# Kernel tuning notes

Measured on AMD Instinct MI355X. Metric: run time of the kernel, lower is better.

Reference implementation:

```python
import jax, jax.numpy as jnp
import numpy as np

NUM_TAGS = 128
NUM_FEATURES = 500000
B, T, F = 64, 512, 8


def setup_inputs() -> dict:
    key = jax.random.key(0)
    ks = jax.random.split(key, 6)
    feats = jax.random.randint(ks[0], (B, T, F), 0, NUM_FEATURES)
    tags = jax.random.randint(ks[1], (B, T), 0, NUM_TAGS)
    # original init: uniform(-0.01, 0.01)
    state_weights = jax.random.uniform(ks[2], (NUM_TAGS, NUM_FEATURES), minval=-0.01, maxval=0.01, dtype=jnp.float32)
    transitions = jax.random.uniform(ks[3], (NUM_TAGS, NUM_TAGS), minval=-0.01, maxval=0.01, dtype=jnp.float32)
    start_transitions = jax.random.uniform(ks[4], (NUM_TAGS,), minval=-0.01, maxval=0.01, dtype=jnp.float32)
    end_transitions = jax.random.uniform(ks[5], (NUM_TAGS,), minval=-0.01, maxval=0.01, dtype=jnp.float32)
    return dict(feats=feats, tags=tags, state_weights=state_weights,
                transitions=transitions, start_transitions=start_transitions,
                end_transitions=end_transitions)


def reference(feats, tags, state_weights, transitions, start_transitions, end_transitions):
    """Batched CRF negative log-likelihood per sentence: logZ - gold_score. Returns [B]."""
    # emissions[b,t,k] = sum_f state_weights[k, feats[b,t,f]]  (emissions_for_sentence)
    emissions = jnp.take(state_weights, feats, axis=1).sum(-1)   # [K,B,T]
    emissions = jnp.moveaxis(emissions, 0, -1)                    # [B,T,K]

    # log_partition: forward algorithm over T via scan
    alpha0 = start_transitions[None, :] + emissions[:, 0]         # [B,K]

    def step(alpha, em_t):
        # scores[b,i,j] = alpha[b,i] + transitions[i,j]
        scores = alpha[:, :, None] + transitions[None, :, :]
        return jax.nn.logsumexp(scores, axis=1) + em_t, None

    em_rest = jnp.moveaxis(emissions[:, 1:], 1, 0)                # [T-1,B,K]
    alphaT, _ = jax.lax.scan(step, alpha0, em_rest)
    log_z = jax.nn.logsumexp(alphaT + end_transitions[None, :], axis=1)   # [B]

    # gold_score, vectorized over batch
    em_gold = jnp.take_along_axis(emissions, tags[..., None], axis=2)[..., 0].sum(axis=1)  # [B]
    trans_gold = transitions[tags[:, :-1], tags[:, 1:]].sum(axis=1)                        # [B]
    gold = start_transitions[tags[:, 0]] + end_transitions[tags[:, -1]] + em_gold + trans_gold

    return log_z - gold
```

## Files before the change

### kernel.cpp

```cpp
#include <hip/hip_runtime.h>

#define NUM_TAGS 128
#define NUM_FEATS 500000
#define BB 64
#define TT 512
#define FF 8

#define SWT_BYTES 128000000ull
#define EM_BYTES  16777216ull
#define NEED_FULL (SWT_BYTES + EM_BYTES)

typedef __attribute__((ext_vector_type(8))) short short8;
typedef __attribute__((ext_vector_type(4))) float float4v;

__device__ inline unsigned short f2bf(float f) {
  unsigned u = __float_as_uint(f);
  return (unsigned short)((u + 0x7fffu + ((u >> 16) & 1u)) >> 16);
}
__device__ inline float bf2f(unsigned short h) {
  return __uint_as_float(((unsigned)h) << 16);
}

__global__ __launch_bounds__(256) void transpose_kernel(
    const float* __restrict__ sw, unsigned short* __restrict__ swT) {
  __shared__ float tile[32][129];
  const int f0 = blockIdx.x * 32;
  const int t = threadIdx.x;
  const int fi = t & 31, kb = t >> 5;
#pragma unroll
  for (int it = 0; it < 16; ++it) {
    int k = kb + it * 8;
    tile[fi][k] = sw[(size_t)k * NUM_FEATS + f0 + fi];
  }
  __syncthreads();
  const int kp = (t & 63) * 2, fo = t >> 6;
#pragma unroll
  for (int it = 0; it < 8; ++it) {
    int f2 = fo + it * 4;
    unsigned v = (unsigned)f2bf(tile[f2][kp]) |
                 ((unsigned)f2bf(tile[f2][kp + 1]) << 16);
    *(unsigned*)&swT[(size_t)(f0 + f2) * NUM_TAGS + kp] = v;
  }
}

__global__ __launch_bounds__(128) void gather_t_kernel(
    const int* __restrict__ feats, const unsigned short* __restrict__ swT,
    float* __restrict__ em_exp) {
  const int token = blockIdx.x;
  const int k = threadIdx.x;
  const int* f = feats + token * FF;
  float s = 0.f;
#pragma unroll
  for (int i = 0; i < FF; ++i) s += bf2f(swT[(size_t)f[i] * NUM_TAGS + k]);
  em_exp[(size_t)token * NUM_TAGS + k] = __expf(s);
}

__global__ __launch_bounds__(128) void gather_f_kernel(
    const int* __restrict__ feats, const float* __restrict__ sw,
    float* __restrict__ em_exp) {
  const int token = blockIdx.x;
  const int k = threadIdx.x;
  const int* f = feats + token * FF;
  const float* row = sw + (size_t)k * NUM_FEATS;
  float s = 0.f;
#pragma unroll
  for (int i = 0; i < FF; ++i) s += row[f[i]];
  em_exp[(size_t)token * NUM_TAGS + k] = __expf(s);
}

#define NB 16
#define LROW 136
#define LBUF (NB * LROW)

__global__ __launch_bounds__(256, 1) void fwd_kernel(
    const float* __restrict__ em_exp, const int* __restrict__ tags,
    const float* __restrict__ trans, const float* __restrict__ startT,
    const float* __restrict__ endT, float* __restrict__ out) {
  __shared__ __align__(16) unsigned short abuf[2][LBUF];
  __shared__ float red[16][17];

  const int tid = threadIdx.x;
  const int bl = tid & 15;
  const int h = (tid >> 4) & 3;
  const int w = tid >> 6;
  const int bg = blockIdx.x * NB + bl;

  short8 afrag[2][4];
#pragma unroll
  for (int mt = 0; mt < 2; ++mt) {
    const int j = (2 * w + mt) * 16 + bl;
#pragma unroll
    for (int kc = 0; kc < 4; ++kc) {
      short8 a;
#pragma unroll
      for (int jj = 0; jj < 8; ++jj) {
        int i = kc * 32 + h * 8 + jj;
        a[jj] = (short)f2bf(__expf(trans[i * NUM_TAGS + j]) * 0.0078125f);
      }
      afrag[mt][kc] = a;
    }
  }

  const float* emb = em_exp + (size_t)bg * TT * NUM_TAGS;

  {
    const int jc = tid >> 4, j0 = jc * 8;
#pragma unroll
    for (int jj = 0; jj < 8; ++jj)
      abuf[0][bl * LROW + j0 + jj] =
          f2bf(__expf(startT[j0 + jj]) * emb[j0 + jj]);
  }
  __syncthreads();

  float4v ev[2];
#pragma unroll
  for (int mt = 0; mt < 2; ++mt) {
    int j0 = (2 * w + mt) * 16 + h * 4;
    ev[mt] = *(const float4v*)&emb[(size_t)NUM_TAGS + j0];
  }

  for (int t = 1; t < TT; ++t) {
    const unsigned short* cur = abuf[(t - 1) & 1];
    unsigned short* nxt = abuf[t & 1];

    short8 bfrag[4];
#pragma unroll
    for (int kc = 0; kc < 4; ++kc)
      bfrag[kc] = *(const short8*)&cur[bl * LROW + kc * 32 + h * 8];

    float4v acc0 = {0.f, 0.f, 0.f, 0.f}, acc1 = {0.f, 0.f, 0.f, 0.f};
#pragma unroll
    for (int kc = 0; kc < 4; ++kc) {
      acc0 = __builtin_amdgcn_mfma_f32_16x16x32_bf16(afrag[0][kc], bfrag[kc], acc0, 0, 0, 0);
      acc1 = __builtin_amdgcn_mfma_f32_16x16x32_bf16(afrag[1][kc], bfrag[kc], acc1, 0, 0, 0);
    }

    float4v e0 = ev[0], e1 = ev[1];
    if (t + 1 < TT) {
#pragma unroll
      for (int mt = 0; mt < 2; ++mt) {
        int j0 = (2 * w + mt) * 16 + h * 4;
        ev[mt] = *(const float4v*)&emb[(size_t)(t + 1) * NUM_TAGS + j0];
      }
    }
    {
      int j0 = (2 * w + 0) * 16 + h * 4;
      uint2 u;
      u.x = (unsigned)f2bf(acc0[0] * e0[0]) | ((unsigned)f2bf(acc0[1] * e0[1]) << 16);
      u.y = (unsigned)f2bf(acc0[2] * e0[2]) | ((unsigned)f2bf(acc0[3] * e0[3]) << 16);
      *(uint2*)&nxt[bl * LROW + j0] = u;
    }
    {
      int j0 = (2 * w + 1) * 16 + h * 4;
      uint2 u;
      u.x = (unsigned)f2bf(acc1[0] * e1[0]) | ((unsigned)f2bf(acc1[1] * e1[1]) << 16);
      u.y = (unsigned)f2bf(acc1[2] * e1[2]) | ((unsigned)f2bf(acc1[3] * e1[3]) << 16);
      *(uint2*)&nxt[bl * LROW + j0] = u;
    }
    __syncthreads();
  }

  {
    const int jc = tid >> 4, j0 = jc * 8;
    const unsigned short* fin = abuf[(TT - 1) & 1];
    float val = 0.f;
#pragma unroll
    for (int jj = 0; jj < 8; ++jj)
      val += bf2f(fin[bl * LROW + j0 + jj]) * __expf(endT[j0 + jj]);
    red[jc][bl] = val;
  }
  __syncthreads();
  float logzv = 0.f;
  if (tid < 16) {
    float s = 0.f;
#pragma unroll
    for (int q = 0; q < 16; ++q) s += red[q][tid];
    logzv = __logf(s) + 511.0f * 7.0f * 0.69314718055994531f;
  }
  __syncthreads();

  {
    const int seg = tid >> 4;
    const int* tb = tags + (size_t)bg * TT;
    float g = 0.f;
    for (int t = seg * 32; t < seg * 32 + 32; ++t) {
      int tg = tb[t];
      g += __logf(emb[(size_t)t * NUM_TAGS + tg]);
      if (t < TT - 1) g += trans[tg * NUM_TAGS + tb[t + 1]];
    }
    if (seg == 0) g += startT[tb[0]];
    if (seg == 15) g += endT[tb[TT - 1]];
    red[seg][bl] = g;
  }
  __syncthreads();
  if (tid < 16) {
    float s = 0.f;
#pragma unroll
    for (int q = 0; q < 16; ++q) s += red[q][tid];
    out[blockIdx.x * NB + tid] = logzv - s;
  }
}

extern "C" void kernel_launch(void* const* d_in, const int* in_sizes, int n_in,
                              void* d_out, int out_size, void* d_ws, size_t ws_size,
                              hipStream_t stream) {
  const int* feats = (const int*)d_in[0];
  const int* tags = (const int*)d_in[1];
  const float* sw = (const float*)d_in[2];
  const float* trans = (const float*)d_in[3];
  const float* startT = (const float*)d_in[4];
  const float* endT = (const float*)d_in[5];
  float* out = (float*)d_out;

  if (ws_size >= NEED_FULL) {
    unsigned short* swT = (unsigned short*)d_ws;
    float* em_exp = (float*)((char*)d_ws + SWT_BYTES);
    transpose_kernel<<<NUM_FEATS / 32, 256, 0, stream>>>(sw, swT);
    gather_t_kernel<<<BB * TT, 128, 0, stream>>>(feats, swT, em_exp);
    fwd_kernel<<<BB / NB, 256, 0, stream>>>(em_exp, tags, trans, startT, endT, out);
  } else {
    float* em_exp = (float*)d_ws;
    gather_f_kernel<<<BB * TT, 128, 0, stream>>>(feats, sw, em_exp);
    fwd_kernel<<<BB / NB, 256, 0, stream>>>(em_exp, tags, trans, startT, endT, out);
  }
}
```

Measured before the change: 633.9 us.

## Store emissions as bf16, precompute gold score in gather, widen transpose tiles

Emission storage moves from fp32 to bf16, which halves the traffic for writing and reading the emission buffer. The gold emission term is now taken from the raw sums inside the gather kernel, and a separate small kernel computes the gold transition term, so the serial forward kernel no longer does log lookups at the end. The transpose kernel switches to 128-feature tiles with float4 loads and converts to bf16 before staging in LDS. The gather kernel packs two tags per lane with 8 tokens per block, and the forward loop uses a cheaper bf16 rounding built on perm, which adds a little precision loss.

```diff
diff --git a/kernel.cpp b/kernel.cpp
--- a/kernel.cpp
+++ b/kernel.cpp
@@ -7,8 +7,10 @@
 #define FF 8
 
 #define SWT_BYTES 128000000ull
-#define EM_BYTES  16777216ull
-#define NEED_FULL (SWT_BYTES + EM_BYTES)
+#define EM_BYTES  (64ull * 512 * 128 * 2)
+#define GEP_BYTES (4096ull * 4)
+#define GTR_BYTES (64ull * 4)
+#define NEED_FULL (SWT_BYTES + EM_BYTES + GEP_BYTES + GTR_BYTES)
 
 typedef __attribute__((ext_vector_type(8))) short short8;
 typedef __attribute__((ext_vector_type(4))) float float4v;
@@ -21,69 +23,141 @@
   return __uint_as_float(((unsigned)h) << 16);
 }
 
+__global__ __launch_bounds__(256) void gold_trans_kernel(
+    const int* __restrict__ tags, const float* __restrict__ trans,
+    const float* __restrict__ startT, const float* __restrict__ endT,
+    float* __restrict__ gold_tr) {
+  const int b = blockIdx.x;
+  const int* tb = tags + (size_t)b * TT;
+  float g = 0.f;
+  for (int t = threadIdx.x; t < TT - 1; t += 256)
+    g += trans[tb[t] * NUM_TAGS + tb[t + 1]];
+  if (threadIdx.x == 0) g += startT[tb[0]] + endT[tb[TT - 1]];
+#pragma unroll
+  for (int m = 32; m > 0; m >>= 1) g += __shfl_xor(g, m, 64);
+  __shared__ float r[4];
+  if ((threadIdx.x & 63) == 0) r[threadIdx.x >> 6] = g;
+  __syncthreads();
+  if (threadIdx.x == 0) gold_tr[b] = r[0] + r[1] + r[2] + r[3];
+}
+
 __global__ __launch_bounds__(256) void transpose_kernel(
     const float* __restrict__ sw, unsigned short* __restrict__ swT) {
-  __shared__ float tile[32][129];
-  const int f0 = blockIdx.x * 32;
+#define TS 136
+  __shared__ unsigned short tile[128 * TS];
+  const int f0 = blockIdx.x * 128;
   const int t = threadIdx.x;
-  const int fi = t & 31, kb = t >> 5;
-#pragma unroll
-  for (int it = 0; it < 16; ++it) {
-    int k = kb + it * 8;
-    tile[fi][k] = sw[(size_t)k * NUM_FEATS + f0 + fi];
-  }
-  __syncthreads();
-  const int kp = (t & 63) * 2, fo = t >> 6;
-#pragma unroll
-  for (int it = 0; it < 8; ++it) {
-    int f2 = fo + it * 4;
-    unsigned v = (unsigned)f2bf(tile[f2][kp]) |
-                 ((unsigned)f2bf(tile[f2][kp + 1]) << 16);
-    *(unsigned*)&swT[(size_t)(f0 + f2) * NUM_TAGS + kp] = v;
-  }
-}
-
-__global__ __launch_bounds__(128) void gather_t_kernel(
+  const int c = t & 31, kr = t >> 5;
+#pragma unroll
+  for (int p = 0; p < 16; ++p) {
+    int k = kr + 8 * p;
+    int f = f0 + 4 * c;
+    if (f < NUM_FEATS) {
+      float4 v = *(const float4*)&sw[(size_t)k * NUM_FEATS + f];
+      uint2 o;
+      o.x = (unsigned)f2bf(v.x) | ((unsigned)f2bf(v.y) << 16);
+      o.y = (unsigned)f2bf(v.z) | ((unsigned)f2bf(v.w) << 16);
+      *(uint2*)&tile[k * TS + 4 * c] = o;
+    }
+  }
+  __syncthreads();
+  const int c2 = t & 31, fr = t >> 5;
+#pragma unroll
+  for (int p = 0; p < 16; ++p) {
+    int f = fr + 8 * p;
+    if (f0 + f < NUM_FEATS) {
+      uint2 o;
+      o.x = (unsigned)tile[(4 * c2 + 0) * TS + f] |
+            ((unsigned)tile[(4 * c2 + 1) * TS + f] << 16);
+      o.y = (unsigned)tile[(4 * c2 + 2) * TS + f] |
+            ((unsigned)tile[(4 * c2 + 3) * TS + f] << 16);
+      *(uint2*)&swT[(size_t)(f0 + f) * NUM_TAGS + 4 * c2] = o;
+    }
+  }
+#undef TS
+}
+
+__global__ __launch_bounds__(512) void gather_kernel(
     const int* __restrict__ feats, const unsigned short* __restrict__ swT,
-    float* __restrict__ em_exp) {
-  const int token = blockIdx.x;
-  const int k = threadIdx.x;
-  const int* f = feats + token * FF;
-  float s = 0.f;
-#pragma unroll
-  for (int i = 0; i < FF; ++i) s += bf2f(swT[(size_t)f[i] * NUM_TAGS + k]);
-  em_exp[(size_t)token * NUM_TAGS + k] = __expf(s);
-}
-
-__global__ __launch_bounds__(128) void gather_f_kernel(
+    unsigned short* __restrict__ em, const int* __restrict__ tags,
+    float* __restrict__ gold_ep) {
+  const int w = threadIdx.x >> 6, lane = threadIdx.x & 63;
+  const int token = blockIdx.x * 8 + w;
+  const int* f = feats + (size_t)token * FF;
+  float s0 = 0.f, s1 = 0.f;
+#pragma unroll
+  for (int i = 0; i < FF; ++i) {
+    unsigned u = *(const unsigned*)&swT[(size_t)f[i] * NUM_TAGS + 2 * lane];
+    s0 += __uint_as_float(u << 16);
+    s1 += __uint_as_float(u & 0xFFFF0000u);
+  }
+  unsigned lo = f2bf(__expf(s0));
+  unsigned hi = f2bf(__expf(s1));
+  *(unsigned*)&em[(size_t)token * NUM_TAGS + 2 * lane] = lo | (hi << 16);
+
+  int tg = tags[token];
+  float c = (2 * lane == tg) ? s0 : ((2 * lane + 1 == tg) ? s1 : 0.f);
+#pragma unroll
+  for (int m = 32; m > 0; m >>= 1) c += __shfl_xor(c, m, 64);
+  __shared__ float part[8];
+  if (lane == 0) part[w] = c;
+  __syncthreads();
+  if (threadIdx.x == 0) {
+    float s = 0.f;
+#pragma unroll
+    for (int i = 0; i < 8; ++i) s += part[i];
+    gold_ep[blockIdx.x] = s;
+  }
+}
+
+__global__ __launch_bounds__(512) void gather_f_kernel(
     const int* __restrict__ feats, const float* __restrict__ sw,
-    float* __restrict__ em_exp) {
-  const int token = blockIdx.x;
-  const int k = threadIdx.x;
-  const int* f = feats + token * FF;
-  const float* row = sw + (size_t)k * NUM_FEATS;
-  float s = 0.f;
-#pragma unroll
-  for (int i = 0; i < FF; ++i) s += row[f[i]];
-  em_exp[(size_t)token * NUM_TAGS + k] = __expf(s);
+    unsigned short* __restrict__ em, const int* __restrict__ tags,
+    float* __restrict__ gold_ep) {
+  const int w = threadIdx.x >> 6, lane = threadIdx.x & 63;
+  const int token = blockIdx.x * 8 + w;
+  const int* f = feats + (size_t)token * FF;
+  float s0 = 0.f, s1 = 0.f;
+#pragma unroll
+  for (int i = 0; i < FF; ++i) {
+    s0 += sw[(size_t)(2 * lane) * NUM_FEATS + f[i]];
+    s1 += sw[(size_t)(2 * lane + 1) * NUM_FEATS + f[i]];
+  }
+  unsigned lo = f2bf(__expf(s0));
+  unsigned hi = f2bf(__expf(s1));
+  *(unsigned*)&em[(size_t)token * NUM_TAGS + 2 * lane] = lo | (hi << 16);
+
+  int tg = tags[token];
+  float c = (2 * lane == tg) ? s0 : ((2 * lane + 1 == tg) ? s1 : 0.f);
+#pragma unroll
+  for (int m = 32; m > 0; m >>= 1) c += __shfl_xor(c, m, 64);
+  __shared__ float part[8];
+  if (lane == 0) part[w] = c;
+  __syncthreads();
+  if (threadIdx.x == 0) {
+    float s = 0.f;
+#pragma unroll
+    for (int i = 0; i < 8; ++i) s += part[i];
+    gold_ep[blockIdx.x] = s;
+  }
 }
 
 #define NB 16
 #define LROW 136
-#define LBUF (NB * LROW)
 
 __global__ __launch_bounds__(256, 1) void fwd_kernel(
-    const float* __restrict__ em_exp, const int* __restrict__ tags,
-    const float* __restrict__ trans, const float* __restrict__ startT,
-    const float* __restrict__ endT, float* __restrict__ out) {
-  __shared__ __align__(16) unsigned short abuf[2][LBUF];
+    const unsigned short* __restrict__ em, const float* __restrict__ trans,
+    const float* __restrict__ startT, const float* __restrict__ endT,
+    const float* __restrict__ gold_tr, const float* __restrict__ gold_ep,
+    float* __restrict__ out) {
+  __shared__ __align__(16) unsigned short alds[2][NB * LROW];
   __shared__ float red[16][17];
+  __shared__ float redz[16];
 
   const int tid = threadIdx.x;
-  const int bl = tid & 15;
-  const int h = (tid >> 4) & 3;
-  const int w = tid >> 6;
-  const int bg = blockIdx.x * NB + bl;
+  const int w = tid >> 6, lane = tid & 63;
+  const int bl = lane & 15, h = lane >> 4;
+  const int b0 = blockIdx.x * NB;
 
   short8 afrag[2][4];
 #pragma unroll
@@ -101,27 +175,35 @@
     }
   }
 
-  const float* emb = em_exp + (size_t)bg * TT * NUM_TAGS;
+  const unsigned short* emb = em + (size_t)(b0 + bl) * TT * NUM_TAGS;
 
   {
-    const int jc = tid >> 4, j0 = jc * 8;
-#pragma unroll
-    for (int jj = 0; jj < 8; ++jj)
-      abuf[0][bl * LROW + j0 + jj] =
-          f2bf(__expf(startT[j0 + jj]) * emb[j0 + jj]);
-  }
-  __syncthreads();
-
-  float4v ev[2];
-#pragma unroll
-  for (int mt = 0; mt < 2; ++mt) {
-    int j0 = (2 * w + mt) * 16 + h * 4;
-    ev[mt] = *(const float4v*)&emb[(size_t)NUM_TAGS + j0];
-  }
+    const int bl2 = tid & 15, jc = tid >> 4;
+    const unsigned short* e2 = em + (size_t)(b0 + bl2) * TT * NUM_TAGS;
+#pragma unroll
+    for (int jj = 0; jj < 8; ++jj) {
+      int j = jc * 8 + jj;
+      alds[0][bl2 * LROW + j] = f2bf(__expf(startT[j]) * bf2f(e2[j]));
+    }
+  }
+  __syncthreads();
+
+  uint2 ev[2];
+#pragma unroll
+  for (int mt = 0; mt < 2; ++mt)
+    ev[mt] = *(const uint2*)&emb[(size_t)NUM_TAGS + (2 * w + mt) * 16 + 4 * h];
 
   for (int t = 1; t < TT; ++t) {
-    const unsigned short* cur = abuf[(t - 1) & 1];
-    unsigned short* nxt = abuf[t & 1];
+    uint2 evn[2];
+    if (t + 1 < TT) {
+#pragma unroll
+      for (int mt = 0; mt < 2; ++mt)
+        evn[mt] = *(const uint2*)&emb[(size_t)(t + 1) * NUM_TAGS +
+                                      (2 * w + mt) * 16 + 4 * h];
+    }
+
+    const unsigned short* cur = alds[(t - 1) & 1];
+    unsigned short* nxt = alds[t & 1];
 
     short8 bfrag[4];
 #pragma unroll
@@ -135,69 +217,57 @@
       acc1 = __builtin_amdgcn_mfma_f32_16x16x32_bf16(afrag[1][kc], bfrag[kc], acc1, 0, 0, 0);
     }
 
-    float4v e0 = ev[0], e1 = ev[1];
-    if (t + 1 < TT) {
-#pragma unroll
-      for (int mt = 0; mt < 2; ++mt) {
-        int j0 = (2 * w + mt) * 16 + h * 4;
-        ev[mt] = *(const float4v*)&emb[(size_t)(t + 1) * NUM_TAGS + j0];
-      }
-    }
-    {
-      int j0 = (2 * w + 0) * 16 + h * 4;
-      uint2 u;
-      u.x = (unsigned)f2bf(acc0[0] * e0[0]) | ((unsigned)f2bf(acc0[1] * e0[1]) << 16);
-      u.y = (unsigned)f2bf(acc0[2] * e0[2]) | ((unsigned)f2bf(acc0[3] * e0[3]) << 16);
-      *(uint2*)&nxt[bl * LROW + j0] = u;
-    }
-    {
-      int j0 = (2 * w + 1) * 16 + h * 4;
-      uint2 u;
-      u.x = (unsigned)f2bf(acc1[0] * e1[0]) | ((unsigned)f2bf(acc1[1] * e1[1]) << 16);
-      u.y = (unsigned)f2bf(acc1[2] * e1[2]) | ((unsigned)f2bf(acc1[3] * e1[3]) << 16);
-      *(uint2*)&nxt[bl * LROW + j0] = u;
-    }
+#pragma unroll
+    for (int mt = 0; mt < 2; ++mt) {
+      const float4v& A = mt ? acc1 : acc0;
+      float e0 = __uint_as_float(ev[mt].x << 16);
+      float e1 = __uint_as_float(ev[mt].x & 0xFFFF0000u);
+      float e2 = __uint_as_float(ev[mt].y << 16);
+      float e3 = __uint_as_float(ev[mt].y & 0xFFFF0000u);
+      unsigned a0 = __float_as_uint(A[0] * e0) + 0x8000u;
+      unsigned a1 = __float_as_uint(A[1] * e1) + 0x8000u;
+      unsigned a2 = __float_as_uint(A[2] * e2) + 0x8000u;
+      unsigned a3 = __float_as_uint(A[3] * e3) + 0x8000u;
+      uint2 o;
+      o.x = __builtin_amdgcn_perm(a1, a0, 0x07060302u);
+      o.y = __builtin_amdgcn_perm(a3, a2, 0x07060302u);
+      *(uint2*)&nxt[bl * LROW + (2 * w + mt) * 16 + 4 * h] = o;
+    }
+    ev[0] = evn[0];
+    ev[1] = evn[1];
     __syncthreads();
   }
 
   {
-    const int jc = tid >> 4, j0 = jc * 8;
-    const unsigned short* fin = abuf[(TT - 1) & 1];
-    float val = 0.f;
-#pragma unroll
-    for (int jj = 0; jj < 8; ++jj)
-      val += bf2f(fin[bl * LROW + j0 + jj]) * __expf(endT[j0 + jj]);
-    red[jc][bl] = val;
-  }
-  __syncthreads();
-  float logzv = 0.f;
+    const int bl2 = tid & 15, jc = tid >> 4;
+    float s = 0.f;
+#pragma unroll
+    for (int jj = 0; jj < 8; ++jj) {
+      int j = jc * 8 + jj;
+      s += bf2f(alds[1][bl2 * LROW + j]) * __expf(endT[j]);
+    }
+    red[jc][bl2] = s;
+  }
+  __syncthreads();
   if (tid < 16) {
     float s = 0.f;
 #pragma unroll
     for (int q = 0; q < 16; ++q) s += red[q][tid];
-    logzv = __logf(s) + 511.0f * 7.0f * 0.69314718055994531f;
+    redz[tid] = __logf(s) + 511.0f * 7.0f * 0.69314718055994531f;
   }
   __syncthreads();
 
   {
-    const int seg = tid >> 4;
-    const int* tb = tags + (size_t)bg * TT;
-    float g = 0.f;
-    for (int t = seg * 32; t < seg * 32 + 32; ++t) {
-      int tg = tb[t];
-      g += __logf(emb[(size_t)t * NUM_TAGS + tg]);
-      if (t < TT - 1) g += trans[tg * NUM_TAGS + tb[t + 1]];
-    }
-    if (seg == 0) g += startT[tb[0]];
-    if (seg == 15) g += endT[tb[TT - 1]];
-    red[seg][bl] = g;
+    const int bl2 = tid & 15, q = tid >> 4;
+    const float* gp = gold_ep + (size_t)(b0 + bl2) * 64 + q * 4;
+    red[q][bl2] = gp[0] + gp[1] + gp[2] + gp[3];
   }
   __syncthreads();
   if (tid < 16) {
-    float s = 0.f;
-#pragma unroll
-    for (int q = 0; q < 16; ++q) s += red[q][tid];
-    out[blockIdx.x * NB + tid] = logzv - s;
+    float g = gold_tr[b0 + tid];
+#pragma unroll
+    for (int q = 0; q < 16; ++q) g += red[q][tid];
+    out[b0 + tid] = redz[tid] - g;
   }
 }
 
@@ -214,13 +284,19 @@
 
   if (ws_size >= NEED_FULL) {
     unsigned short* swT = (unsigned short*)d_ws;
-    float* em_exp = (float*)((char*)d_ws + SWT_BYTES);
-    transpose_kernel<<<NUM_FEATS / 32, 256, 0, stream>>>(sw, swT);
-    gather_t_kernel<<<BB * TT, 128, 0, stream>>>(feats, swT, em_exp);
-    fwd_kernel<<<BB / NB, 256, 0, stream>>>(em_exp, tags, trans, startT, endT, out);
+    unsigned short* em = (unsigned short*)((char*)d_ws + SWT_BYTES);
+    float* gold_ep = (float*)((char*)d_ws + SWT_BYTES + EM_BYTES);
+    float* gold_tr = (float*)((char*)d_ws + SWT_BYTES + EM_BYTES + GEP_BYTES);
+    gold_trans_kernel<<<BB, 256, 0, stream>>>(tags, trans, startT, endT, gold_tr);
+    transpose_kernel<<<(NUM_FEATS + 127) / 128, 256, 0, stream>>>(sw, swT);
+    gather_kernel<<<BB * TT / 8, 512, 0, stream>>>(feats, swT, em, tags, gold_ep);
+    fwd_kernel<<<BB / NB, 256, 0, stream>>>(em, trans, startT, endT, gold_tr, gold_ep, out);
   } else {
-    float* em_exp = (float*)d_ws;
-    gather_f_kernel<<<BB * TT, 128, 0, stream>>>(feats, sw, em_exp);
-    fwd_kernel<<<BB / NB, 256, 0, stream>>>(em_exp, tags, trans, startT, endT, out);
-  }
-}
+    unsigned short* em = (unsigned short*)d_ws;
+    float* gold_ep = (float*)((char*)d_ws + EM_BYTES);
+    float* gold_tr = (float*)((char*)d_ws + EM_BYTES + GEP_BYTES);
+    gold_trans_kernel<<<BB, 256, 0, stream>>>(tags, trans, startT, endT, gold_tr);
+    gather_f_kernel<<<BB * TT / 8, 512, 0, stream>>>(feats, sw, em, tags, gold_ep);
+    fwd_kernel<<<BB / NB, 256, 0, stream>>>(em, trans, startT, endT, gold_tr, gold_ep, out);
+  }
+}
```

New measurement: 578.3 us. 8.8% less time.
